# Kernel optimization log

Measured on AMD Instinct MI355X. Metric: run time of the kernel, lower is better.

Reference implementation:

```python
import jax, jax.numpy as jnp
import numpy as np

N, IN_DIM, OUT_DIM = 8192, 512, 256
ALPHA = 0.2  # LeakyReLU negative slope
MASK_VAL = -9e15


def setup_inputs() -> dict:
    key = jax.random.key(0)
    k1, k2, k3, k4 = jax.random.split(key, 4)
    inp = jax.random.normal(k1, (N, IN_DIM), dtype=jnp.float32)
    adj = jax.random.randint(k2, (N, N), 0, 2, dtype=jnp.int32)
    # xavier-ish scaled params
    weight = jax.random.normal(k3, (IN_DIM, OUT_DIM), dtype=jnp.float32) * (2.0 / (IN_DIM + OUT_DIM)) ** 0.5
    a = jax.random.normal(k4, (2 * OUT_DIM, 1), dtype=jnp.float32) * (2.0 / (2 * OUT_DIM + 1)) ** 0.5
    return {"input": inp, "adj": adj, "weight": weight, "a": a}


def reference(input, adj, weight, a):
    Wh = input @ weight                        # [N, D_out]
    Wh1 = Wh @ a[:OUT_DIM, :]                  # [N, 1]
    Wh2 = Wh @ a[OUT_DIM:, :]                  # [N, 1]
    e = Wh1 + Wh2.T                            # [N, N] broadcast additive score
    e = jnp.where(e > 0, e, ALPHA * e)         # LeakyReLU
    e = jnp.where(adj > 0, e, MASK_VAL)        # adjacency mask
    attention = jax.nn.softmax(e, axis=-1)     # [N, N]
    # dropout p=0.0 -> identity
    out = attention @ Wh                       # [N, D_out]
    return jax.nn.elu(out)
```

## Files before the change

### kernel.cpp

```cpp
#include <hip/hip_runtime.h>
#include <hip/hip_bf16.h>
#include <stdint.h>

#define NN 8192
#define DIN 512
#define DOUT 256
#define NSPLIT 8
#define STRIP (NN / NSPLIT)
#define KVBLK 64
#define NSTEP (STRIP / KVBLK)
#define LOG2E 1.4426950408889634f

typedef short short8 __attribute__((ext_vector_type(8)));
typedef float floatx4 __attribute__((ext_vector_type(4)));

__device__ __forceinline__ unsigned short f2bf_rne(float x) {
  unsigned u = __float_as_uint(x);
  u += 0x7fffu + ((u >> 16) & 1u);
  return (unsigned short)(u >> 16);
}

__device__ __forceinline__ unsigned cvt_pk_bf16(float lo, float hi) {
  unsigned r;
  asm("v_cvt_pk_bf16_f32 %0, %1, %2" : "=v"(r) : "v"(lo), "v"(hi));
  return r;
}

__global__ __launch_bounds__(256) void kt_transpose(const float* __restrict__ Wg,
                                                    unsigned short* __restrict__ WT) {
  __shared__ unsigned short sm[32][33];
  int tid = threadIdx.x;
  int bk = blockIdx.x >> 3;
  int bn = blockIdx.x & 7;
  int k0 = bk * 32, n0 = bn * 32;
  int r = tid >> 3, c4 = (tid & 7) * 4;
  const float* src = Wg + (size_t)(k0 + r) * DOUT + n0 + c4;
#pragma unroll
  for (int x = 0; x < 4; ++x) sm[r][c4 + x] = f2bf_rne(src[x]);
  __syncthreads();
  unsigned short* dst = WT + (size_t)(n0 + r) * DIN + k0 + c4;
#pragma unroll
  for (int x = 0; x < 4; ++x) dst[x] = sm[c4 + x][r];
}

__global__ __launch_bounds__(256) void kt_cvtx(const float* __restrict__ X,
                                               unsigned short* __restrict__ Xb) {
  int g = blockIdx.x * 256 + threadIdx.x;
  const float4* p = (const float4*)(X + (size_t)g * 8);
  float4 a = p[0], b = p[1];
  union { unsigned u[4]; short8 s8; } r;
  r.u[0] = cvt_pk_bf16(a.x, a.y);
  r.u[1] = cvt_pk_bf16(a.z, a.w);
  r.u[2] = cvt_pk_bf16(b.x, b.y);
  r.u[3] = cvt_pk_bf16(b.z, b.w);
  *(short8*)(Xb + (size_t)g * 8) = r.s8;
}

__global__ __launch_bounds__(256, 2) void kt_gemm1(const unsigned short* __restrict__ Xb,
                                                   const unsigned short* __restrict__ WT,
                                                   const float* __restrict__ Ab,
                                                   unsigned short* __restrict__ WhT,
                                                   float* __restrict__ Wh1,
                                                   float* __restrict__ Wh2) {
  __shared__ __align__(16) unsigned short xs[64 * DIN];
  int tid = threadIdx.x;
  int w = tid >> 6, lane = tid & 63;
  int col = lane & 15, q = lane >> 4;
  int ib = blockIdx.x & 127;
  int db = blockIdx.x >> 7;
  int i0 = ib * 64;

  int sr = tid >> 2, sc = tid & 3, sxor = sr & 7;
  const unsigned short* gX = Xb + (size_t)(i0 + sr) * DIN + sc * 8;
  unsigned short* lX = xs + sr * DIN;
  short8 stg[8];
#pragma unroll
  for (int n = 0; n < 8; ++n) stg[n] = *(const short8*)(gX + n * 32);
#pragma unroll
  for (int n = 0; n < 8; ++n) {
    int l = sc + n * 4;
    *(short8*)(lX + ((l ^ sxor) * 8)) = stg[n];
  }
#pragma unroll
  for (int n = 8; n < 16; ++n) stg[n - 8] = *(const short8*)(gX + n * 32);
#pragma unroll
  for (int n = 8; n < 16; ++n) {
    int l = sc + n * 4;
    *(short8*)(lX + ((l ^ sxor) * 8)) = stg[n - 8];
  }

  int drow = db * 64 + w * 16 + col;
  const unsigned short* abase = WT + (size_t)drow * DIN + q * 8;
  short8 af[16];
#pragma unroll
  for (int s = 0; s < 16; ++s) af[s] = *(const short8*)(abase + s * 32);

  __syncthreads();

  floatx4 acc[4];
#pragma unroll
  for (int t = 0; t < 4; ++t) acc[t] = (floatx4)(0.0f);
  int cx = col & 7;
#pragma unroll
  for (int s = 0; s < 16; ++s) {
#pragma unroll
    for (int t = 0; t < 4; ++t) {
      short8 bf = *(const short8*)(xs + (t * 16 + col) * DIN + (((s * 4 + q) ^ cx) * 8));
      acc[t] = __builtin_amdgcn_mfma_f32_16x16x32_bf16(af[s], bf, acc[t], 0, 0, 0);
    }
  }

  int dq = db * 64 + w * 16 + q * 4;
  float a1v[4], a2v[4];
#pragma unroll
  for (int r = 0; r < 4; ++r) {
    a1v[r] = Ab[dq + r] * LOG2E;
    a2v[r] = Ab[DOUT + dq + r] * LOG2E;
  }
#pragma unroll
  for (int t = 0; t < 4; ++t) {
    floatx4 v = acc[t];
    int icol = i0 + t * 16 + col;
#pragma unroll
    for (int r = 0; r < 4; ++r) WhT[(size_t)(dq + r) * NN + icol] = f2bf_rne(v[r]);
    float p1 = v[0] * a1v[0] + v[1] * a1v[1] + v[2] * a1v[2] + v[3] * a1v[3];
    float p2 = v[0] * a2v[0] + v[1] * a2v[1] + v[2] * a2v[2] + v[3] * a2v[3];
    p1 += __shfl_xor(p1, 16);
    p1 += __shfl_xor(p1, 32);
    p2 += __shfl_xor(p2, 16);
    p2 += __shfl_xor(p2, 32);
    if (q == 0) {
      atomicAdd(&Wh1[icol], p1);
      atomicAdd(&Wh2[icol], p2);
    }
  }
}

__device__ __forceinline__ short8 build_a(int4 pa, int4 pb, float wh1, floatx4 w2a,
                                          floatx4 w2b, float& lsum) {
  int av[8] = {pa.x, pa.y, pa.z, pa.w, pb.x, pb.y, pb.z, pb.w};
  float w2[8] = {w2a[0], w2a[1], w2a[2], w2a[3], w2b[0], w2b[1], w2b[2], w2b[3]};
  float wv[8];
#pragma unroll
  for (int e = 0; e < 8; ++e) {
    float sc = wh1 + w2[e];
    sc = fmaxf(sc, 0.2f * sc);
    float ex = __builtin_amdgcn_exp2f(sc);
    wv[e] = (av[e] != 0) ? ex : 0.0f;
  }
  union { unsigned u[4]; short8 s8; } r;
#pragma unroll
  for (int p = 0; p < 4; ++p) {
    unsigned pk = cvt_pk_bf16(wv[2 * p], wv[2 * p + 1]);
    r.u[p] = pk;
    lsum += __uint_as_float(pk << 16) + __uint_as_float(pk & 0xffff0000u);
  }
  return r.s8;
}

__global__ __launch_bounds__(256, 2) void kt_attn(const int* __restrict__ adj,
                                                  const unsigned short* __restrict__ WhT,
                                                  const float* __restrict__ Wh1,
                                                  const float* __restrict__ Wh2,
                                                  float* __restrict__ accs,
                                                  float* __restrict__ lgp) {
  __shared__ __align__(16) unsigned short tileB[2][DOUT * KVBLK];
  __shared__ __align__(16) float wh2s[STRIP];
  int tid = threadIdx.x;
  int w = tid >> 6, lane = tid & 63;
  int col = lane & 15, q = lane >> 4;
  int s = blockIdx.x & (NSPLIT - 1);
  int ib = blockIdx.x >> 3;
  int i0 = ib * 128;
  int jb = s * STRIP;

  ((float4*)wh2s)[tid] = ((const float4*)(Wh2 + jb))[tid];

  int r0 = i0 + w * 32 + col;
  float wh1r0 = Wh1[r0];
  float wh1r1 = Wh1[r0 + 16];

  int sw = tid & 7;
  const unsigned short* gsrc = WhT + (size_t)tid * NN + jb;
  unsigned short* lrow0 = &tileB[0][tid * KVBLK];

  int ck = col & 7;
  int off0 = col * KVBLK + ((q ^ ck) * 8);
  int off1 = col * KVBLK + (((4 + q) ^ ck) * 8);
  const unsigned short* tb0 = &tileB[0][0];

  const int* aptr0 = adj + ((size_t)r0 << 13) + jb + q * 8;
  const int* aptr1 = adj + ((size_t)(r0 + 16) << 13) + jb + q * 8;

  floatx4 acc0[16], acc1[16];
#pragma unroll
  for (int t = 0; t < 16; ++t) {
    acc0[t] = (floatx4)(0.0f);
    acc1[t] = (floatx4)(0.0f);
  }
  float lp0 = 0.f, lp1 = 0.f;

  short8 st[8];
#pragma unroll
  for (int n = 0; n < 8; ++n) st[n] = *(const short8*)(gsrc + n * 8);
  int4 aA0a = *(const int4*)aptr0;
  int4 aA0b = *(const int4*)(aptr0 + 4);
  int4 aA1a = *(const int4*)aptr1;
  int4 aA1b = *(const int4*)(aptr1 + 4);
  int4 aB0a = *(const int4*)(aptr0 + 32);
  int4 aB0b = *(const int4*)(aptr0 + 36);
  int4 aB1a = *(const int4*)(aptr1 + 32);
  int4 aB1b = *(const int4*)(aptr1 + 36);

#pragma unroll 1
  for (int k = 0; k < NSTEP; ++k) {
    int bsel = (k & 1) * (DOUT * KVBLK);
    unsigned short* lw = lrow0 + bsel;
#pragma unroll
    for (int n = 0; n < 8; ++n) *(short8*)(lw + ((n ^ sw) * 8)) = st[n];
    if (k + 1 < NSTEP) {
      const unsigned short* gs = gsrc + (size_t)(k + 1) * KVBLK;
#pragma unroll
      for (int n = 0; n < 8; ++n) st[n] = *(const short8*)(gs + n * 8);
    }
    asm volatile("s_waitcnt lgkmcnt(0)\ns_barrier" ::: "memory");
    int jl = k * KVBLK;
    {
      floatx4 w2a = *(const floatx4*)&wh2s[jl + q * 8];
      floatx4 w2b = *(const floatx4*)&wh2s[jl + q * 8 + 4];
      short8 af0 = build_a(aA0a, aA0b, wh1r0, w2a, w2b, lp0);
      short8 af1 = build_a(aA1a, aA1b, wh1r1, w2a, w2b, lp1);
      if (k + 1 < NSTEP) {
        int jn = (k + 1) * KVBLK;
        aA0a = *(const int4*)(aptr0 + jn);
        aA0b = *(const int4*)(aptr0 + jn + 4);
        aA1a = *(const int4*)(aptr1 + jn);
        aA1b = *(const int4*)(aptr1 + jn + 4);
      }
      const unsigned short* br = tb0 + bsel + off0;
#pragma unroll
      for (int h = 0; h < 4; ++h) {
        short8 bf[4];
#pragma unroll
        for (int t = 0; t < 4; ++t) bf[t] = *(const short8*)(br + (h * 4 + t) * 1024);
#pragma unroll
        for (int t = 0; t < 4; ++t) {
          acc0[h * 4 + t] =
              __builtin_amdgcn_mfma_f32_16x16x32_bf16(af0, bf[t], acc0[h * 4 + t], 0, 0, 0);
          acc1[h * 4 + t] =
              __builtin_amdgcn_mfma_f32_16x16x32_bf16(af1, bf[t], acc1[h * 4 + t], 0, 0, 0);
        }
      }
    }
    {
      floatx4 w2a = *(const floatx4*)&wh2s[jl + 32 + q * 8];
      floatx4 w2b = *(const floatx4*)&wh2s[jl + 32 + q * 8 + 4];
      short8 ag0 = build_a(aB0a, aB0b, wh1r0, w2a, w2b, lp0);
      short8 ag1 = build_a(aB1a, aB1b, wh1r1, w2a, w2b, lp1);
      if (k + 1 < NSTEP) {
        int jn = (k + 1) * KVBLK + 32;
        aB0a = *(const int4*)(aptr0 + jn);
        aB0b = *(const int4*)(aptr0 + jn + 4);
        aB1a = *(const int4*)(aptr1 + jn);
        aB1b = *(const int4*)(aptr1 + jn + 4);
      }
      const unsigned short* br = tb0 + bsel + off1;
#pragma unroll
      for (int h = 0; h < 4; ++h) {
        short8 bf[4];
#pragma unroll
        for (int t = 0; t < 4; ++t) bf[t] = *(const short8*)(br + (h * 4 + t) * 1024);
#pragma unroll
        for (int t = 0; t < 4; ++t) {
          acc0[h * 4 + t] =
              __builtin_amdgcn_mfma_f32_16x16x32_bf16(ag0, bf[t], acc0[h * 4 + t], 0, 0, 0);
          acc1[h * 4 + t] =
              __builtin_amdgcn_mfma_f32_16x16x32_bf16(ag1, bf[t], acc1[h * 4 + t], 0, 0, 0);
        }
      }
    }
  }

  lp0 += __shfl_xor(lp0, 16);
  lp0 += __shfl_xor(lp0, 32);
  lp1 += __shfl_xor(lp1, 16);
  lp1 += __shfl_xor(lp1, 32);
  if (lane < 16) {
    __builtin_nontemporal_store(lp0, &lgp[(size_t)s * NN + i0 + w * 32 + lane]);
    __builtin_nontemporal_store(lp1, &lgp[(size_t)s * NN + i0 + w * 32 + 16 + lane]);
  }
  float* slab = accs + (size_t)s * NN * DOUT;
#pragma unroll
  for (int T = 0; T < 16; ++T) {
    floatx4 v0 = acc0[T];
    floatx4 v1 = acc1[T];
    int dcol = T * 16 + col;
    int irow0 = i0 + w * 32 + q * 4;
#pragma unroll
    for (int r = 0; r < 4; ++r)
      __builtin_nontemporal_store(v0[r], &slab[(size_t)(irow0 + r) * DOUT + dcol]);
#pragma unroll
    for (int r = 0; r < 4; ++r)
      __builtin_nontemporal_store(v1[r], &slab[(size_t)(irow0 + 16 + r) * DOUT + dcol]);
  }
}

__global__ __launch_bounds__(256) void kt_merge(const float* __restrict__ accs,
                                                const float* __restrict__ lgp,
                                                float* __restrict__ out) {
  int g = blockIdx.x * 256 + threadIdx.x;
  int i = g >> 6;
  float l = 0.f;
#pragma unroll
  for (int s = 0; s < NSPLIT; ++s) l += lgp[(size_t)s * NN + i];
  float4 a = *(const float4*)(accs + (size_t)g * 4);
#pragma unroll
  for (int s = 1; s < NSPLIT; ++s) {
    float4 b = *(const float4*)(accs + (size_t)s * NN * DOUT + (size_t)g * 4);
    a.x += b.x; a.y += b.y; a.z += b.z; a.w += b.w;
  }
  float inv = 1.0f / l;
  float o[4] = {a.x * inv, a.y * inv, a.z * inv, a.w * inv};
#pragma unroll
  for (int r = 0; r < 4; ++r) o[r] = o[r] > 0.f ? o[r] : (__expf(o[r]) - 1.f);
  *(float4*)(out + (size_t)g * 4) = make_float4(o[0], o[1], o[2], o[3]);
}

extern "C" void kernel_launch(void* const* d_in, const int* in_sizes, int n_in,
                              void* d_out, int out_size, void* d_ws, size_t ws_size,
                              hipStream_t stream) {
  const float* X = (const float*)d_in[0];
  const int* adj = (const int*)d_in[1];
  const float* Wg = (const float*)d_in[2];
  const float* Ab = (const float*)d_in[3];
  float* out = (float*)d_out;

  char* ws = (char*)d_ws;
  float* accs = (float*)ws;
  unsigned short* Xb = (unsigned short*)ws;
  size_t off = (size_t)NSPLIT * NN * DOUT * 4;
  float* lgp = (float*)(ws + off);
  off += (size_t)NSPLIT * NN * 4;
  float* Wh1 = (float*)(ws + off);
  off += (size_t)NN * 4;
  float* Wh2 = (float*)(ws + off);
  off += (size_t)NN * 4;
  unsigned short* WT = (unsigned short*)(ws + off);
  off += (size_t)DOUT * DIN * 2;
  unsigned short* WhT = (unsigned short*)(ws + off);
  off += (size_t)DOUT * NN * 2;

  hipMemsetAsync(Wh1, 0, (size_t)NN * 8, stream);
  kt_cvtx<<<2048, 256, 0, stream>>>(X, Xb);
  kt_transpose<<<128, 256, 0, stream>>>(Wg, WT);
  kt_gemm1<<<512, 256, 0, stream>>>(Xb, WT, Ab, WhT, Wh1, Wh2);
  kt_attn<<<(NN / 128) * NSPLIT, 256, 0, stream>>>(adj, WhT, Wh1, Wh2, accs, lgp);
  kt_merge<<<2048, 256, 0, stream>>>(accs, lgp, out);
}
```

Baseline: 442.3 us.

## Store Wh transposed in 32-column blocked layout for contiguous attention tile loads

gemm1 now writes the bf16 transposed Wh into a blocked layout: 32-node chunks, each holding all 256 feature rows of 32 contiguous elements. The attention kernel's B-tile staging loads are rewritten to match, so each 64-column step reads two contiguous 16 KB blocks instead of 256 strided rows. The LDS swizzle offsets are adjusted to the new thread-to-row mapping. The aim is better global load coalescing and fewer DRAM/TLB pages touched per tile. The cost is more scattered stores in gemm1.

```diff
diff --git a/kernel.cpp b/kernel.cpp
--- a/kernel.cpp
+++ b/kernel.cpp
@@ -59,7 +59,7 @@
 __global__ __launch_bounds__(256, 2) void kt_gemm1(const unsigned short* __restrict__ Xb,
                                                    const unsigned short* __restrict__ WT,
                                                    const float* __restrict__ Ab,
-                                                   unsigned short* __restrict__ WhT,
+                                                   unsigned short* __restrict__ WhTb,
                                                    float* __restrict__ Wh1,
                                                    float* __restrict__ Wh2) {
   __shared__ __align__(16) unsigned short xs[64 * DIN];
@@ -122,7 +122,8 @@
     floatx4 v = acc[t];
     int icol = i0 + t * 16 + col;
 #pragma unroll
-    for (int r = 0; r < 4; ++r) WhT[(size_t)(dq + r) * NN + icol] = f2bf_rne(v[r]);
+    for (int r = 0; r < 4; ++r)
+      WhTb[((size_t)(icol >> 5) * DOUT + (dq + r)) * 32 + (icol & 31)] = f2bf_rne(v[r]);
     float p1 = v[0] * a1v[0] + v[1] * a1v[1] + v[2] * a1v[2] + v[3] * a1v[3];
     float p2 = v[0] * a2v[0] + v[1] * a2v[1] + v[2] * a2v[2] + v[3] * a2v[3];
     p1 += __shfl_xor(p1, 16);
@@ -159,7 +160,7 @@
 }
 
 __global__ __launch_bounds__(256, 2) void kt_attn(const int* __restrict__ adj,
-                                                  const unsigned short* __restrict__ WhT,
+                                                  const unsigned short* __restrict__ WhTb,
                                                   const float* __restrict__ Wh1,
                                                   const float* __restrict__ Wh2,
                                                   float* __restrict__ accs,
@@ -180,9 +181,12 @@
   float wh1r0 = Wh1[r0];
   float wh1r1 = Wh1[r0 + 16];
 
-  int sw = tid & 7;
-  const unsigned short* gsrc = WhT + (size_t)tid * NN + jb;
-  unsigned short* lrow0 = &tileB[0][tid * KVBLK];
+  const unsigned short* gW = WhTb + (size_t)(s * 32) * 8192 + tid * 8;
+  int scn = tid & 3, sx = (tid >> 2) & 7;
+  unsigned short* lrow0 = &tileB[0][(tid >> 2) * KVBLK];
+  int wo[2];
+  wo[0] = ((scn ^ sx) * 8);
+  wo[1] = (((4 + scn) ^ sx) * 8);
 
   int ck = col & 7;
   int off0 = col * KVBLK + ((q ^ ck) * 8);
@@ -202,7 +206,10 @@
 
   short8 st[8];
 #pragma unroll
-  for (int n = 0; n < 8; ++n) st[n] = *(const short8*)(gsrc + n * 8);
+  for (int n = 0; n < 2; ++n)
+#pragma unroll
+    for (int m = 0; m < 4; ++m)
+      st[n * 4 + m] = *(const short8*)(gW + n * 8192 + m * 2048);
   int4 aA0a = *(const int4*)aptr0;
   int4 aA0b = *(const int4*)(aptr0 + 4);
   int4 aA1a = *(const int4*)aptr1;
@@ -217,11 +224,17 @@
     int bsel = (k & 1) * (DOUT * KVBLK);
     unsigned short* lw = lrow0 + bsel;
 #pragma unroll
-    for (int n = 0; n < 8; ++n) *(short8*)(lw + ((n ^ sw) * 8)) = st[n];
+    for (int n = 0; n < 2; ++n)
+#pragma unroll
+      for (int m = 0; m < 4; ++m)
+        *(short8*)(lw + m * (64 * KVBLK) + wo[n]) = st[n * 4 + m];
     if (k + 1 < NSTEP) {
-      const unsigned short* gs = gsrc + (size_t)(k + 1) * KVBLK;
-#pragma unroll
-      for (int n = 0; n < 8; ++n) st[n] = *(const short8*)(gs + n * 8);
+      const unsigned short* gs = gW + (size_t)(2 * (k + 1)) * 8192;
+#pragma unroll
+      for (int n = 0; n < 2; ++n)
+#pragma unroll
+        for (int m = 0; m < 4; ++m)
+          st[n * 4 + m] = *(const short8*)(gs + n * 8192 + m * 2048);
     }
     asm volatile("s_waitcnt lgkmcnt(0)\ns_barrier" ::: "memory");
     int jl = k * KVBLK;
@@ -347,13 +360,13 @@
   off += (size_t)NN * 4;
   unsigned short* WT = (unsigned short*)(ws + off);
   off += (size_t)DOUT * DIN * 2;
-  unsigned short* WhT = (unsigned short*)(ws + off);
+  unsigned short* WhTb = (unsigned short*)(ws + off);
   off += (size_t)DOUT * NN * 2;
 
   hipMemsetAsync(Wh1, 0, (size_t)NN * 8, stream);
   kt_cvtx<<<2048, 256, 0, stream>>>(X, Xb);
   kt_transpose<<<128, 256, 0, stream>>>(Wg, WT);
-  kt_gemm1<<<512, 256, 0, stream>>>(Xb, WT, Ab, WhT, Wh1, Wh2);
-  kt_attn<<<(NN / 128) * NSPLIT, 256, 0, stream>>>(adj, WhT, Wh1, Wh2, accs, lgp);
+  kt_gemm1<<<512, 256, 0, stream>>>(Xb, WT, Ab, WhTb, Wh1, Wh2);
+  kt_attn<<<(NN / 128) * NSPLIT, 256, 0, stream>>>(adj, WhTb, Wh1, Wh2, accs, lgp);
   kt_merge<<<2048, 256, 0, stream>>>(accs, lgp, out);
 }
```

Result: no change. 445.2 us (+0.6%).
